# Kernel optimization log

Hardware: AMD Instinct MI355X
Metric: run time of the kernel (lower is better)

## Reference

```python
import jax, jax.numpy as jnp
import numpy as np

B, T, C = 8, 2048, 1024  # micro_bsz, seq_len, n_embd (== complexsize)


def setup_inputs() -> dict:
    key = jax.random.key(0)
    ks = jax.random.split(key, 6)
    w = lambda k, shape: (jax.random.normal(k, shape, dtype=jnp.float32) * 0.02)
    return {
        "x": jax.random.normal(ks[0], (B, T, C), dtype=jnp.float32),
        "Wk": w(ks[1], (2 * C, C)),      # key: n_embd -> 2*n_embd (no bias)
        "Wa": w(ks[2], (C, 2 * C)),      # activation: 2*n_embd -> n_embd (no bias)
        "Wf": w(ks[3], (2, C, C)),       # WaveNet filter conv, kernel=2, WIO layout
        "Wg": w(ks[4], (2, C, C)),       # WaveNet gate conv, kernel=2, WIO layout
        "Wo": w(ks[5], (C, C)),          # WaveNet 1x1 output projection
    }


def _causal_conv(x, W):
    # x: [B,T,Cin], W: [K,Cin,Cout]; left-pad K-1 for causality
    return jax.lax.conv_general_dilated(
        x, W, window_strides=(1,), padding=[(W.shape[0] - 1, 0)],
        dimension_numbers=("NWC", "WIO", "NWC"))


def _wavenet_short(x, Wf, Wg, Wo):
    # undialated gated WaveNet unit: tanh(conv_f(x)) * sigmoid(conv_g(x)) -> 1x1 proj
    h = jnp.tanh(_causal_conv(x, Wf)) * jax.nn.sigmoid(_causal_conv(x, Wg))
    return h @ Wo.T


def reference(x, Wk, Wa, Wf, Wg, Wo):
    Bx, Tx, Cx = x.shape
    k = (x @ Wk.T).reshape(Bx, Tx, Cx, 2)                 # [B,T,C,2]
    cv = jax.lax.complex(k[..., 0], k[..., 1])            # view_as_complex -> [B,T,C]
    scale = jax.lax.cummax(jnp.abs(cv), axis=1)           # running max of magnitude
    cv2 = cv / scale.astype(cv.dtype)                      # normalize magnitude <= 1
    kv = jnp.cumprod(cv2, axis=1)                          # complex cumulative product
    re = jnp.stack([kv.real, kv.imag], axis=-1).reshape(Bx, Tx, 2 * Cx)  # view_as_real
    return (re @ Wa.T) * _wavenet_short(x * scale, Wf, Wg, Wo)
```

## Files before the change

kernel.cpp:

```cpp
#include <hip/hip_runtime.h>
#include <cmath>

#define T_SEQ 2048
#define C_DIM 1024
#define BM 128
#define BN 128
#define BK 32

typedef unsigned short u16;
typedef unsigned int u32;
typedef short bf16x8 __attribute__((ext_vector_type(8)));
typedef _Float16 f16x8 __attribute__((ext_vector_type(8)));
typedef float f32x4 __attribute__((ext_vector_type(4)));
typedef unsigned short u16x8 __attribute__((ext_vector_type(8)));

#define AS1 __attribute__((address_space(1)))
#define AS3 __attribute__((address_space(3)))

__device__ __forceinline__ u16 f2bf(float f) {
    u32 u = __builtin_bit_cast(u32, f);
    u32 r = u + 0x7fffu + ((u >> 16) & 1u);
    return (u16)(r >> 16);
}
__device__ __forceinline__ u16 f2h(float f) {
    return __builtin_bit_cast(u16, (_Float16)f);
}
__device__ __forceinline__ float h2f(u16 h) {
    return (float)__builtin_bit_cast(_Float16, h);
}
__device__ __forceinline__ void gl_lds16(const void* g, void* l) {
    __builtin_amdgcn_global_load_lds((const AS1 u32*)g, (AS3 u32*)l, 16, 0, 0);
}

__device__ __forceinline__ int xcd_swz(int lin, int nwg) {
    return (lin & 7) * (nwg >> 3) + (lin >> 3);
}

template<int EPI, int DT>
__global__ __launch_bounds__(256)
void mfma_gemm(const u16* __restrict__ Ap, const u16* __restrict__ B0,
               void* __restrict__ Cout, int M, int N, int K)
{
    __shared__ u16 lds[2 * 2 * 4096];
    const int tid  = threadIdx.x;
    const int lane = tid & 63;
    const int wid  = tid >> 6;
    const int wr = wid >> 1, wc = wid & 1;
    const int gx = gridDim.x;
    const int lin = xcd_swz(blockIdx.x + gx * blockIdx.y, gx * gridDim.y);
    const int m0 = (lin / gx) * BM;
    const int n0 = (lin % gx) * BN;
    const int NT = K / BK;

    f32x4 acc[4][4] = {};

    auto stage = [&](int it, int buf) {
        const int k0 = it * BK;
        u16* base = &lds[buf * 8192];
        #pragma unroll
        for (int i = 0; i < 2; ++i) {
            const int chunk = wid + 4 * i;
            const int rloc  = chunk * 16 + (lane >> 2);
            const int slot  = (lane & 3) ^ ((rloc >> 1) & 3);
            gl_lds16(B0 + (size_t)(n0 + rloc) * K + k0 + slot * 8,
                     base + 4096 + chunk * 512);
            gl_lds16(Ap + (size_t)(m0 + rloc) * K + k0 + slot * 8,
                     base + chunk * 512);
        }
    };

    auto compute = [&](int buf) {
        const u16* base = &lds[buf * 8192];
        if constexpr (DT == 0) {
            bf16x8 a[4], b[4];
            #pragma unroll
            for (int f = 0; f < 4; ++f) {
                const int row = wr * 64 + f * 16 + (lane & 15);
                const int sp  = ((lane >> 4) & 3) ^ ((row >> 1) & 3);
                a[f] = *(const bf16x8*)&base[row * 32 + sp * 8];
                const int rowb = wc * 64 + f * 16 + (lane & 15);
                const int spb  = ((lane >> 4) & 3) ^ ((rowb >> 1) & 3);
                b[f] = *(const bf16x8*)&base[4096 + rowb * 32 + spb * 8];
            }
            #pragma unroll
            for (int fm = 0; fm < 4; ++fm)
                #pragma unroll
                for (int fn = 0; fn < 4; ++fn)
                    acc[fm][fn] = __builtin_amdgcn_mfma_f32_16x16x32_bf16(a[fm], b[fn], acc[fm][fn], 0, 0, 0);
        } else {
            f16x8 a[4], b[4];
            #pragma unroll
            for (int f = 0; f < 4; ++f) {
                const int row = wr * 64 + f * 16 + (lane & 15);
                const int sp  = ((lane >> 4) & 3) ^ ((row >> 1) & 3);
                a[f] = *(const f16x8*)&base[row * 32 + sp * 8];
                const int rowb = wc * 64 + f * 16 + (lane & 15);
                const int spb  = ((lane >> 4) & 3) ^ ((rowb >> 1) & 3);
                b[f] = *(const f16x8*)&base[4096 + rowb * 32 + spb * 8];
            }
            #pragma unroll
            for (int fm = 0; fm < 4; ++fm)
                #pragma unroll
                for (int fn = 0; fn < 4; ++fn)
                    acc[fm][fn] = __builtin_amdgcn_mfma_f32_16x16x32_f16(a[fm], b[fn], acc[fm][fn], 0, 0, 0);
        }
    };

    stage(0, 0);
    int cur = 0;
    for (int it = 0; it < NT; ++it) {
        __syncthreads();
        if (it + 1 < NT) stage(it + 1, cur ^ 1);
        compute(cur);
        cur ^= 1;
    }

    const int crow0 = m0 + wr * 64 + ((lane >> 4) << 2);
    const int ccol  = n0 + wc * 64 + (lane & 15);
    #pragma unroll
    for (int fm = 0; fm < 4; ++fm)
        #pragma unroll
        for (int fn = 0; fn < 4; ++fn)
            #pragma unroll
            for (int r = 0; r < 4; ++r) {
                const size_t idx = (size_t)(crow0 + fm * 16 + r) * N + ccol + fn * 16;
                if constexpr (EPI == 0) ((float*)Cout)[idx] = acc[fm][fn][r];
                else                    ((u16*)Cout)[idx] = f2h(acc[fm][fn][r]);
            }
}

__global__ __launch_bounds__(256)
void dual_gemm(const u16* __restrict__ A1, const u16* __restrict__ B1, int K1,
               const u16* __restrict__ A2, const u16* __restrict__ B2, int K2,
               float* __restrict__ out, int M, int N)
{
    __shared__ u16 lds[2 * 2 * 4096];
    const int tid  = threadIdx.x;
    const int lane = tid & 63;
    const int wid  = tid >> 6;
    const int wr = wid >> 1, wc = wid & 1;
    const int gx = gridDim.x;
    const int lin = xcd_swz(blockIdx.x + gx * blockIdx.y, gx * gridDim.y);
    const int m0 = (lin / gx) * BM;
    const int n0 = (lin % gx) * BN;

    f32x4 acc1[4][4] = {};
    f32x4 acc2[4][4] = {};

    auto stage = [&](const u16* Ap, const u16* Bp, int K, int it, int buf) {
        const int k0 = it * BK;
        u16* base = &lds[buf * 8192];
        #pragma unroll
        for (int i = 0; i < 2; ++i) {
            const int chunk = wid + 4 * i;
            const int rloc  = chunk * 16 + (lane >> 2);
            const int slot  = (lane & 3) ^ ((rloc >> 1) & 3);
            gl_lds16(Bp + (size_t)(n0 + rloc) * K + k0 + slot * 8,
                     base + 4096 + chunk * 512);
            gl_lds16(Ap + (size_t)(m0 + rloc) * K + k0 + slot * 8,
                     base + chunk * 512);
        }
    };

    auto compute = [&](int buf, f32x4 (&acc)[4][4]) {
        const u16* base = &lds[buf * 8192];
        bf16x8 a[4], b[4];
        #pragma unroll
        for (int f = 0; f < 4; ++f) {
            const int row = wr * 64 + f * 16 + (lane & 15);
            const int sp  = ((lane >> 4) & 3) ^ ((row >> 1) & 3);
            a[f] = *(const bf16x8*)&base[row * 32 + sp * 8];
            const int rowb = wc * 64 + f * 16 + (lane & 15);
            const int spb  = ((lane >> 4) & 3) ^ ((rowb >> 1) & 3);
            b[f] = *(const bf16x8*)&base[4096 + rowb * 32 + spb * 8];
        }
        #pragma unroll
        for (int fm = 0; fm < 4; ++fm)
            #pragma unroll
            for (int fn = 0; fn < 4; ++fn)
                acc[fm][fn] = __builtin_amdgcn_mfma_f32_16x16x32_bf16(a[fm], b[fn], acc[fm][fn], 0, 0, 0);
    };

    const int NT1 = K1 / BK, NT2 = K2 / BK;
    stage(A1, B1, K1, 0, 0);
    int cur = 0;
    for (int it = 0; it < NT1; ++it) {
        __syncthreads();
        if (it + 1 < NT1) stage(A1, B1, K1, it + 1, cur ^ 1);
        else              stage(A2, B2, K2, 0, cur ^ 1);
        compute(cur, acc1);
        cur ^= 1;
    }
    for (int it = 0; it < NT2; ++it) {
        __syncthreads();
        if (it + 1 < NT2) stage(A2, B2, K2, it + 1, cur ^ 1);
        compute(cur, acc2);
        cur ^= 1;
    }

    const int crow0 = m0 + wr * 64 + ((lane >> 4) << 2);
    const int ccol  = n0 + wc * 64 + (lane & 15);
    #pragma unroll
    for (int fm = 0; fm < 4; ++fm)
        #pragma unroll
        for (int fn = 0; fn < 4; ++fn)
            #pragma unroll
            for (int r = 0; r < 4; ++r) {
                const size_t idx = (size_t)(crow0 + fm * 16 + r) * N + ccol + fn * 16;
                out[idx] = acc1[fm][fn][r] * acc2[fm][fn][r];
            }
}

__global__ __launch_bounds__(256)
void conv_gate(const u16* __restrict__ A, const u16* __restrict__ Wfgt,
               u16* __restrict__ H, int M)
{
    constexpr int KIT = C_DIM / BK;
    constexpr int NT  = 2 * KIT;
    __shared__ u16 lds[2 * 3 * 4096];
    const int tid  = threadIdx.x;
    const int lane = tid & 63;
    const int wid  = tid >> 6;
    const int wr = wid >> 1, wc = wid & 1;
    const int gx = gridDim.x;
    const int lin = xcd_swz(blockIdx.x + gx * blockIdx.y, gx * gridDim.y);
    const int m0 = (lin / gx) * BM;
    const int n0 = (lin % gx) * BN;

    f32x4 accF[4][4] = {};
    f32x4 accG[4][4] = {};

    auto stage = [&](int it, int buf) {
        const int p  = it / KIT;
        const int k0 = (it - p * KIT) * BK;
        u16* base = &lds[buf * 12288];
        const u16* BF = Wfgt + (size_t)p * 2 * C_DIM * C_DIM;
        const u16* BG = BF + (size_t)C_DIM * C_DIM;
        const int sh = (p == 0) ? 1 : 0;
        #pragma unroll
        for (int i = 0; i < 2; ++i) {
            const int chunk = wid + 4 * i;
            const int rloc  = chunk * 16 + (lane >> 2);
            const int slot  = (lane & 3) ^ ((rloc >> 1) & 3);
            int grow = m0 + rloc - sh;
            if (grow < 0) grow = 0;
            gl_lds16(A + (size_t)grow * C_DIM + k0 + slot * 8,
                     base + chunk * 512);
            gl_lds16(BF + (size_t)(n0 + rloc) * C_DIM + k0 + slot * 8,
                     base + 4096 + chunk * 512);
            gl_lds16(BG + (size_t)(n0 + rloc) * C_DIM + k0 + slot * 8,
                     base + 8192 + chunk * 512);
        }
    };

    auto compute = [&](int buf) {
        const u16* base = &lds[buf * 12288];
        bf16x8 a[4], bf[4], bg[4];
        #pragma unroll
        for (int f = 0; f < 4; ++f) {
            const int row = wr * 64 + f * 16 + (lane & 15);
            const int sp  = ((lane >> 4) & 3) ^ ((row >> 1) & 3);
            a[f] = *(const bf16x8*)&base[row * 32 + sp * 8];
            const int rowb = wc * 64 + f * 16 + (lane & 15);
            const int spb  = ((lane >> 4) & 3) ^ ((rowb >> 1) & 3);
            bf[f] = *(const bf16x8*)&base[4096 + rowb * 32 + spb * 8];
            bg[f] = *(const bf16x8*)&base[8192 + rowb * 32 + spb * 8];
        }
        #pragma unroll
        for (int fm = 0; fm < 4; ++fm)
            #pragma unroll
            for (int fn = 0; fn < 4; ++fn) {
                accF[fm][fn] = __builtin_amdgcn_mfma_f32_16x16x32_bf16(a[fm], bf[fn], accF[fm][fn], 0, 0, 0);
                accG[fm][fn] = __builtin_amdgcn_mfma_f32_16x16x32_bf16(a[fm], bg[fn], accG[fm][fn], 0, 0, 0);
            }
    };

    stage(0, 0);
    int cur = 0;
    for (int it = 0; it < NT; ++it) {
        __syncthreads();
        if ((it / KIT) == 0 && (m0 % T_SEQ) == 0) {
            if (tid < 4) {
                u16x8 z = {0,0,0,0,0,0,0,0};
                *(u16x8*)&lds[cur * 12288 + tid * 8] = z;
            }
            __syncthreads();
        }
        if (it + 1 < NT) stage(it + 1, cur ^ 1);
        compute(cur);
        cur ^= 1;
    }

    const int crow0 = m0 + wr * 64 + ((lane >> 4) << 2);
    const int ccol  = n0 + wc * 64 + (lane & 15);
    #pragma unroll
    for (int fm = 0; fm < 4; ++fm)
        #pragma unroll
        for (int fn = 0; fn < 4; ++fn)
            #pragma unroll
            for (int r = 0; r < 4; ++r) {
                const float fv = accF[fm][fn][r];
                const float gv = accG[fm][fn][r];
                const float th = 1.0f - 2.0f / (expf(2.0f * fv) + 1.0f);
                const float sg = 1.0f / (1.0f + expf(-gv));
                H[(size_t)(crow0 + fm * 16 + r) * C_DIM + ccol + fn * 16] = f2bf(th * sg);
            }
}

#define SSEG 32
#define SCHB 32
#define SSL (T_SEQ / SSEG)

__global__ __launch_bounds__(1024, 1)
void scan_kernel(u16* __restrict__ kq, u16* __restrict__ xyb)
{
    __shared__ float  lmax[SSEG][SCHB];
    __shared__ float2 lprod[SSEG][SCHB];
    const int blk = blockIdx.x;
    const int b   = blk >> 5;
    const int c0  = (blk & 31) * SCHB;
    const int ch  = threadIdx.x & (SCHB - 1);
    const int seg = threadIdx.x >> 5;
    const int c   = c0 + ch;
    const int t0  = seg * SSL;
    const size_t baseh = (size_t)b * T_SEQ * 2048 + 2 * c + (size_t)t0 * 2048;
    const size_t base1 = (size_t)b * T_SEQ * C_DIM + c + (size_t)t0 * C_DIM;

    float m2 = 0.f;
    {
        size_t idx = baseh;
        for (int t = 0; t < SSL; ++t) {
            const u32 v = *(const u32*)&kq[idx];
            const float re = h2f((u16)(v & 0xffffu));
            const float im = h2f((u16)(v >> 16));
            m2 = fmaxf(m2, re * re + im * im);
            idx += 2048;
        }
    }
    lmax[seg][ch] = sqrtf(m2);
    __syncthreads();
    #pragma unroll
    for (int s = 1; s < SSEG; s <<= 1) {
        const float v = lmax[seg][ch];
        const float u = (seg >= s) ? lmax[seg - s][ch] : 0.f;
        __syncthreads();
        lmax[seg][ch] = fmaxf(v, u);
        __syncthreads();
    }
    const float premax = (seg > 0) ? lmax[seg - 1][ch] : 0.f;

    float pr = 1.f, pi = 0.f;
    float m = premax;
    {
        size_t idx = baseh, idx1 = base1;
        for (int t = 0; t < SSL; ++t) {
            const u32 v = *(const u32*)&kq[idx];
            const float re = h2f((u16)(v & 0xffffu));
            const float im = h2f((u16)(v >> 16));
            m = fmaxf(m, sqrtf(re * re + im * im));
            const float inv = 1.f / m;
            const float r0 = re * inv, r1 = im * inv;
            const float nr = pr * r0 - pi * r1;
            const float ni = pr * r1 + pi * r0;
            pr = nr; pi = ni;
            const float xv = h2f(xyb[idx1]);
            xyb[idx1] = f2bf(xv * m);
            idx += 2048; idx1 += C_DIM;
        }
    }
    lprod[seg][ch] = make_float2(pr, pi);
    __syncthreads();
    #pragma unroll
    for (int s = 1; s < SSEG; s <<= 1) {
        const float2 v = lprod[seg][ch];
        const float2 u = (seg >= s) ? lprod[seg - s][ch] : make_float2(1.f, 0.f);
        __syncthreads();
        lprod[seg][ch] = make_float2(u.x * v.x - u.y * v.y,
                                     u.x * v.y + u.y * v.x);
        __syncthreads();
    }
    float ppr = 1.f, ppi = 0.f;
    if (seg > 0) { const float2 pp = lprod[seg - 1][ch]; ppr = pp.x; ppi = pp.y; }

    pr = 1.f; pi = 0.f;
    m = premax;
    {
        size_t idx = baseh;
        for (int t = 0; t < SSL; ++t) {
            const u32 v = *(const u32*)&kq[idx];
            const float re = h2f((u16)(v & 0xffffu));
            const float im = h2f((u16)(v >> 16));
            m = fmaxf(m, sqrtf(re * re + im * im));
            const float inv = 1.f / m;
            const float r0 = re * inv, r1 = im * inv;
            const float nr = pr * r0 - pi * r1;
            const float ni = pr * r1 + pi * r0;
            pr = nr; pi = ni;
            const float fr = ppr * nr - ppi * ni;
            const float fi = ppr * ni + ppi * nr;
            *(u32*)&kq[idx] = ((u32)f2bf(fi) << 16) | (u32)f2bf(fr);
            idx += 2048;
        }
    }
}

__global__ void cvt_weights(const float* __restrict__ Wk, const float* __restrict__ Wa,
                            const float* __restrict__ Wo, u16* __restrict__ Wkh,
                            u16* __restrict__ Wab, u16* __restrict__ Wob)
{
    const int n1 = 2048 * 1024, n2 = 2 * 2048 * 1024, n3 = n2 + 1024 * 1024;
    const int i = (blockIdx.x * blockDim.x + threadIdx.x) * 4;
    if (i < n1) {
        const float4 v = *(const float4*)&Wk[i];
        ushort4 o; o.x = f2h(v.x); o.y = f2h(v.y); o.z = f2h(v.z); o.w = f2h(v.w);
        *(ushort4*)&Wkh[i] = o;
    } else if (i < n2) {
        const int j = i - n1;
        const float4 v = *(const float4*)&Wa[j];
        ushort4 o; o.x = f2bf(v.x); o.y = f2bf(v.y); o.z = f2bf(v.z); o.w = f2bf(v.w);
        *(ushort4*)&Wab[j] = o;
    } else if (i < n3) {
        const int j = i - n2;
        const float4 v = *(const float4*)&Wo[j];
        ushort4 o; o.x = f2bf(v.x); o.y = f2bf(v.y); o.z = f2bf(v.z); o.w = f2bf(v.w);
        *(ushort4*)&Wob[j] = o;
    }
}

__global__ void cvt_f16(const float* __restrict__ src, u16* __restrict__ dst, int n)
{
    const int i = (blockIdx.x * blockDim.x + threadIdx.x) * 4;
    if (i >= n) return;
    const float4 v = *(const float4*)&src[i];
    ushort4 o;
    o.x = f2h(v.x); o.y = f2h(v.y); o.z = f2h(v.z); o.w = f2h(v.w);
    *(ushort4*)&dst[i] = o;
}

__global__ __launch_bounds__(256)
void wtrans(const float* __restrict__ Wf, const float* __restrict__ Wg,
            u16* __restrict__ dst)
{
    __shared__ float tile[64][65];
    const int z = blockIdx.z;
    const float* src = ((z < 2) ? Wf : Wg) + (size_t)(z & 1) * C_DIM * C_DIM;
    u16* d = dst + (size_t)(z & 1) * (2 * C_DIM) * C_DIM
                 + ((z < 2) ? (size_t)0 : (size_t)C_DIM * C_DIM);
    const int k0 = blockIdx.x * 64;
    const int n0 = blockIdx.y * 64;
    const int tx = threadIdx.x & 63, ty = threadIdx.x >> 6;
    #pragma unroll
    for (int i = 0; i < 16; ++i) {
        const int r = ty + i * 4;
        tile[r][tx] = src[(size_t)(k0 + r) * C_DIM + n0 + tx];
    }
    __syncthreads();
    #pragma unroll
    for (int i = 0; i < 16; ++i) {
        const int r = ty + i * 4;
        d[(size_t)(n0 + r) * C_DIM + k0 + tx] = f2bf(tile[tx][r]);
    }
}

extern "C" void kernel_launch(void* const* d_in, const int* in_sizes, int n_in,
                              void* d_out, int out_size, void* d_ws, size_t ws_size,
                              hipStream_t stream)
{
    const float* x  = (const float*)d_in[0];
    const float* Wk = (const float*)d_in[1];
    const float* Wa = (const float*)d_in[2];
    const float* Wf = (const float*)d_in[3];
    const float* Wg = (const float*)d_in[4];
    const float* Wo = (const float*)d_in[5];
    float* out = (float*)d_out;

    const int M = 8 * T_SEQ;
    u16* kq   = (u16*)d_ws;
    u16* yb   = (u16*)((char*)d_ws + 67108864ull);
    u16* hb   = (u16*)((char*)d_ws + 100663296ull);
    u16* Wkh  = (u16*)((char*)d_ws + 134217728ull);
    u16* Wab  = Wkh + 2048 * 1024;
    u16* Wfgt = Wab + 2048 * 1024;
    u16* Wob  = Wfgt + 2ull * 2048 * 1024;

    cvt_weights<<<(5 * 1024 * 1024 / 4 + 255) / 256, 256, 0, stream>>>(
        Wk, Wa, Wo, Wkh, Wab, Wob);
    wtrans  <<<dim3(16, 16, 4), 256, 0, stream>>>(Wf, Wg, Wfgt);
    cvt_f16 <<<(M * 1024 / 4) / 256, 256, 0, stream>>>(x, yb, M * 1024);

    mfma_gemm<2, 1><<<dim3(2048 / BN, M / BM), 256, 0, stream>>>(
        yb, Wkh, kq, M, 2048, 1024);

    scan_kernel<<<256, 1024, 0, stream>>>(kq, yb);

    conv_gate<<<dim3(1024 / BN, M / BM), 256, 0, stream>>>(yb, Wfgt, hb, M);

    dual_gemm<<<dim3(1024 / BN, M / BM), 256, 0, stream>>>(
        kq, Wab, 2048, hb, Wob, 1024, out, M, 1024);
}
```

Baseline: 463.8 us.

## Replace key GEMM with 256x256-tile, 8-wave pipelined MFMA kernel

Swaps the 128x128 two-buffer GEMM used for the x@Wk projection for a new kernel with 256x256 tiles, 512 threads and BK=64. The kernel splits each K step into four quarter-stage loads, interleaves them with MFMA groups using explicit vmcnt waits and barriers, and raises wave priority around the MFMA blocks. The goal is more data reuse per LDS byte and better overlap of global loads with compute. In exchange it uses more LDS and registers per block and launches fewer blocks.

```diff
diff --git a/kernel.cpp b/kernel.cpp
--- a/kernel.cpp
+++ b/kernel.cpp
@@ -36,97 +36,110 @@
     return (lin & 7) * (nwg >> 3) + (lin >> 3);
 }
 
-template<int EPI, int DT>
-__global__ __launch_bounds__(256)
-void mfma_gemm(const u16* __restrict__ Ap, const u16* __restrict__ B0,
-               void* __restrict__ Cout, int M, int N, int K)
-{
-    __shared__ u16 lds[2 * 2 * 4096];
+#define SBAR() do { __builtin_amdgcn_sched_barrier(0); \
+                    __builtin_amdgcn_s_barrier(); \
+                    __builtin_amdgcn_sched_barrier(0); } while (0)
+#define VMC(n) do { asm volatile("s_waitcnt vmcnt(" #n ")" ::: "memory"); \
+                    __builtin_amdgcn_sched_barrier(0); } while (0)
+
+__global__ __launch_bounds__(512, 2)
+void gemm8(const u16* __restrict__ Ap, const u16* __restrict__ Bp,
+           u16* __restrict__ Cout, int M, int N, int K)
+{
+    __shared__ u16 lds[2 * 32768];
     const int tid  = threadIdx.x;
     const int lane = tid & 63;
     const int wid  = tid >> 6;
-    const int wr = wid >> 1, wc = wid & 1;
+    const int wrow = wid >> 2;
+    const int wcol = wid & 3;
     const int gx = gridDim.x;
     const int lin = xcd_swz(blockIdx.x + gx * blockIdx.y, gx * gridDim.y);
-    const int m0 = (lin / gx) * BM;
-    const int n0 = (lin % gx) * BN;
-    const int NT = K / BK;
-
-    f32x4 acc[4][4] = {};
-
-    auto stage = [&](int it, int buf) {
-        const int k0 = it * BK;
-        u16* base = &lds[buf * 8192];
-        #pragma unroll
-        for (int i = 0; i < 2; ++i) {
-            const int chunk = wid + 4 * i;
-            const int rloc  = chunk * 16 + (lane >> 2);
-            const int slot  = (lane & 3) ^ ((rloc >> 1) & 3);
-            gl_lds16(B0 + (size_t)(n0 + rloc) * K + k0 + slot * 8,
-                     base + 4096 + chunk * 512);
-            gl_lds16(Ap + (size_t)(m0 + rloc) * K + k0 + slot * 8,
-                     base + chunk * 512);
-        }
-    };
-
-    auto compute = [&](int buf) {
-        const u16* base = &lds[buf * 8192];
-        if constexpr (DT == 0) {
-            bf16x8 a[4], b[4];
+    const int m0 = (lin / gx) * 256;
+    const int n0 = (lin % gx) * 256;
+    const int NT = K / 64;
+
+    f32x4 acc[8][4] = {};
+
+    auto stageu = [&](int t, int u) {
+        const int isB = u & 1, kh = u >> 1;
+        u16* ubase = &lds[(t & 1) * 32768 + isB * 16384 + kh * 8192];
+        const u16* src = isB ? Bp + (size_t)n0 * K : Ap + (size_t)m0 * K;
+        const int k0 = t * 64 + kh * 32;
+        #pragma unroll
+        for (int j = 0; j < 2; ++j) {
+            const int c = wid + 8 * j;
+            const int p = c * 64 + lane;
+            const int row = p >> 2;
+            const int sp  = (p & 3) ^ ((row >> 1) & 3);
+            gl_lds16(src + (size_t)row * K + k0 + sp * 8, ubase + c * 512);
+        }
+    };
+
+    auto lda = [&](int buf, int kh, int mq, f16x8 (&a)[4]) {
+        const u16* base = &lds[buf * 32768 + kh * 8192];
+        #pragma unroll
+        for (int f = 0; f < 4; ++f) {
+            const int row = wrow * 128 + mq * 64 + f * 16 + (lane & 15);
+            const int sp  = (lane >> 4) ^ ((row >> 1) & 3);
+            a[f] = *(const f16x8*)&base[row * 32 + sp * 8];
+        }
+    };
+    auto ldb = [&](int buf, int kh, f16x8 (&b)[4]) {
+        const u16* base = &lds[buf * 32768 + 16384 + kh * 8192];
+        #pragma unroll
+        for (int f = 0; f < 4; ++f) {
+            const int row = wcol * 64 + f * 16 + (lane & 15);
+            const int sp  = (lane >> 4) ^ ((row >> 1) & 3);
+            b[f] = *(const f16x8*)&base[row * 32 + sp * 8];
+        }
+    };
+    auto mm = [&](const f16x8 (&a)[4], const f16x8 (&b)[4], int mq) {
+        __builtin_amdgcn_s_setprio(1);
+        #pragma unroll
+        for (int fm = 0; fm < 4; ++fm)
             #pragma unroll
-            for (int f = 0; f < 4; ++f) {
-                const int row = wr * 64 + f * 16 + (lane & 15);
-                const int sp  = ((lane >> 4) & 3) ^ ((row >> 1) & 3);
-                a[f] = *(const bf16x8*)&base[row * 32 + sp * 8];
-                const int rowb = wc * 64 + f * 16 + (lane & 15);
-                const int spb  = ((lane >> 4) & 3) ^ ((rowb >> 1) & 3);
-                b[f] = *(const bf16x8*)&base[4096 + rowb * 32 + spb * 8];
-            }
-            #pragma unroll
-            for (int fm = 0; fm < 4; ++fm)
-                #pragma unroll
-                for (int fn = 0; fn < 4; ++fn)
-                    acc[fm][fn] = __builtin_amdgcn_mfma_f32_16x16x32_bf16(a[fm], b[fn], acc[fm][fn], 0, 0, 0);
-        } else {
-            f16x8 a[4], b[4];
-            #pragma unroll
-            for (int f = 0; f < 4; ++f) {
-                const int row = wr * 64 + f * 16 + (lane & 15);
-                const int sp  = ((lane >> 4) & 3) ^ ((row >> 1) & 3);
-                a[f] = *(const f16x8*)&base[row * 32 + sp * 8];
-                const int rowb = wc * 64 + f * 16 + (lane & 15);
-                const int spb  = ((lane >> 4) & 3) ^ ((rowb >> 1) & 3);
-                b[f] = *(const f16x8*)&base[4096 + rowb * 32 + spb * 8];
-            }
-            #pragma unroll
-            for (int fm = 0; fm < 4; ++fm)
-                #pragma unroll
-                for (int fn = 0; fn < 4; ++fn)
-                    acc[fm][fn] = __builtin_amdgcn_mfma_f32_16x16x32_f16(a[fm], b[fn], acc[fm][fn], 0, 0, 0);
-        }
-    };
-
-    stage(0, 0);
-    int cur = 0;
-    for (int it = 0; it < NT; ++it) {
-        __syncthreads();
-        if (it + 1 < NT) stage(it + 1, cur ^ 1);
-        compute(cur);
-        cur ^= 1;
-    }
-
-    const int crow0 = m0 + wr * 64 + ((lane >> 4) << 2);
-    const int ccol  = n0 + wc * 64 + (lane & 15);
-    #pragma unroll
-    for (int fm = 0; fm < 4; ++fm)
+            for (int fn = 0; fn < 4; ++fn)
+                acc[mq * 4 + fm][fn] = __builtin_amdgcn_mfma_f32_16x16x32_f16(
+                    a[fm], b[fn], acc[mq * 4 + fm][fn], 0, 0, 0);
+        __builtin_amdgcn_s_setprio(0);
+    };
+
+    stageu(0, 0); stageu(0, 1); stageu(0, 2); stageu(0, 3);
+    VMC(4);
+    SBAR();
+
+    f16x8 a[4], b[4];
+    for (int t = 0; t < NT; ++t) {
+        const int buf = t & 1;
+        const bool more = (t + 1 < NT);
+        if (more) { stageu(t + 1, 0); VMC(6); } else { VMC(4); }
+        lda(buf, 0, 0, a); ldb(buf, 0, b);
+        mm(a, b, 0);
+        SBAR();
+        if (more) stageu(t + 1, 1);
+        lda(buf, 0, 1, a);
+        mm(a, b, 1);
+        SBAR();
+        if (more) { stageu(t + 1, 2); VMC(6); } else { VMC(0); }
+        lda(buf, 1, 0, a); ldb(buf, 1, b);
+        mm(a, b, 0);
+        SBAR();
+        if (more) stageu(t + 1, 3);
+        lda(buf, 1, 1, a);
+        mm(a, b, 1);
+        SBAR();
+    }
+
+    const int crow0 = m0 + wrow * 128 + ((lane >> 4) << 2);
+    const int ccol  = n0 + wcol * 64 + (lane & 15);
+    #pragma unroll
+    for (int mi = 0; mi < 8; ++mi)
         #pragma unroll
         for (int fn = 0; fn < 4; ++fn)
             #pragma unroll
-            for (int r = 0; r < 4; ++r) {
-                const size_t idx = (size_t)(crow0 + fm * 16 + r) * N + ccol + fn * 16;
-                if constexpr (EPI == 0) ((float*)Cout)[idx] = acc[fm][fn][r];
-                else                    ((u16*)Cout)[idx] = f2h(acc[fm][fn][r]);
-            }
+            for (int r = 0; r < 4; ++r)
+                Cout[(size_t)(crow0 + mi * 16 + r) * N + ccol + fn * 16] =
+                    f2h(acc[mi][fn][r]);
 }
 
 __global__ __launch_bounds__(256)
@@ -488,7 +501,7 @@
     wtrans  <<<dim3(16, 16, 4), 256, 0, stream>>>(Wf, Wg, Wfgt);
     cvt_f16 <<<(M * 1024 / 4) / 256, 256, 0, stream>>>(x, yb, M * 1024);
 
-    mfma_gemm<2, 1><<<dim3(2048 / BN, M / BM), 256, 0, stream>>>(
+    gemm8<<<dim3(2048 / 256, M / 256), 512, 0, stream>>>(
         yb, Wkh, kq, M, 2048, 1024);
 
     scan_kernel<<<256, 1024, 0, stream>>>(kq, yb);
```

Measured after the change: 454.9 us. No clear change (-1.9%).
